# Kernel optimization log

Hardware: AMD Instinct MI355X
Metric: run time of the kernel (lower is better)

Reference implementation:

```python
import jax, jax.numpy as jnp
import numpy as np

ODE_UNFOLDS = 6  # keras-ncp LTCCell default
EPS = 1e-8


def setup_inputs() -> dict:
    dim = 1024
    U = 2 * dim
    B, T = 32, 128
    key = jax.random.key(0)
    ks = jax.random.split(key, 12)
    u = lambda k, shape, lo, hi: jax.random.uniform(k, shape, jnp.float32, lo, hi)
    return {
        "inputs": jax.random.normal(ks[0], (B, T, dim), jnp.float32),
        # per-neuron params (keras-ncp initializer ranges)
        "gleak": u(ks[1], (U,), 0.001, 1.0),
        "vleak": u(ks[2], (U,), -0.2, 0.2),
        "cm": u(ks[3], (U,), 0.4, 0.6),
        # per-synapse params; slot 0 = self synapse, slot 1 = pair synapse (j+dim)%U
        "w": u(ks[4], (U, 2), 0.001, 1.0),
        "sigma": u(ks[5], (U, 2), 3.0, 8.0),
        "mu": u(ks[6], (U, 2), 0.3, 0.8),
        "erev": jnp.full((U, 2), -1.0, jnp.float32),  # internal polarity -1
        # sensory synapse params; each neuron j has one sensory source j%dim
        "sens_w": u(ks[7], (U,), 0.001, 1.0),
        "sens_sigma": u(ks[8], (U,), 3.0, 8.0),
        "sens_mu": u(ks[9], (U,), 0.3, 0.8),
        "sens_erev": jnp.full((U,), 1.0, jnp.float32),  # sensory polarity +1
        # affine input/output maps (LTCCell defaults: ones / zeros)
        "input_w": jnp.ones((dim,), jnp.float32),
        "input_b": jnp.zeros((dim,), jnp.float32),
        "output_w": jnp.ones((dim,), jnp.float32),
        "output_b": jnp.zeros((dim,), jnp.float32),
    }


def reference(inputs, gleak, vleak, cm, w, sigma, mu, erev,
              sens_w, sens_sigma, sens_mu, sens_erev,
              input_w, input_b, output_w, output_b):
    B, T, dim = inputs.shape
    U = 2 * dim
    idx = jnp.arange(U)
    src_idx = jnp.stack([idx, (idx + dim) % U], axis=-1)  # [U,2] recurrent sources per dst
    smod = idx % dim                                       # sensory source per dst

    sp_w = jax.nn.softplus(w)          # [U,2]
    sp_sw = jax.nn.softplus(sens_w)    # [U]
    sp_gleak = jax.nn.softplus(gleak)  # [U]
    cm_t = jax.nn.softplus(cm) * ODE_UNFOLDS  # elapsed_time = 1.0

    def step(v, x_t):
        x = x_t * input_w + input_b                                            # [B,dim]
        s_act = sp_sw * jax.nn.sigmoid((x[:, smod] - sens_mu) * sens_sigma)    # [B,U]
        num_s = s_act * sens_erev
        den_s = s_act
        for _ in range(ODE_UNFOLDS):
            va = v[:, src_idx]                                                  # [B,U,2]
            wa = sp_w * jax.nn.sigmoid((va - mu) * sigma)                      # [B,U,2]
            num = jnp.sum(wa * erev, axis=-1) + num_s                          # [B,U]
            den = jnp.sum(wa, axis=-1) + den_s                                 # [B,U]
            v = (cm_t * v + sp_gleak * vleak + num) / (cm_t + sp_gleak + den + EPS)
        return v, None

    v0 = jnp.zeros((B, U), inputs.dtype)
    v_last, _ = jax.lax.scan(step, v0, jnp.swapaxes(inputs, 0, 1))  # scan over time
    return v_last[:, :dim] * output_w + output_b  # motor neurons + affine output map
```

## Files before the change

### kernel.cpp

```cpp
#include <hip/hip_runtime.h>

#define T_STEPS 128
#define DIM 1024
#define ODE_UNFOLDS 6
#define EPS 1e-8f
#define L2E 1.44269504088896340736f

__device__ __forceinline__ float fexp2(float x) { return __builtin_amdgcn_exp2f(x); }
__device__ __forceinline__ float frcp(float x)  { return __builtin_amdgcn_rcpf(x); }

__device__ __forceinline__ float softplus_init(float x) {
  return log2f(1.0f + exp2f(x * L2E)) * (1.0f / L2E);
}

__device__ __forceinline__ float swap_adj(float x) {
  int y = __builtin_amdgcn_mov_dpp(__float_as_int(x), 0xB1, 0xF, 0xF, true);
  return __int_as_float(y);
}

__global__ __launch_bounds__(256) void memcell_kernel(
    const float* __restrict__ inputs,
    const float* __restrict__ gleak,
    const float* __restrict__ vleak,
    const float* __restrict__ cm,
    const float* __restrict__ w,
    const float* __restrict__ sigma,
    const float* __restrict__ mu,
    const float* __restrict__ erev,
    const float* __restrict__ sens_w,
    const float* __restrict__ sens_sigma,
    const float* __restrict__ sens_mu,
    const float* __restrict__ sens_erev,
    const float* __restrict__ input_w,
    const float* __restrict__ input_b,
    const float* __restrict__ output_w,
    const float* __restrict__ output_b,
    float* __restrict__ out)
{
  const int tid  = blockIdx.x * blockDim.x + threadIdx.x;
  const int p    = tid >> 1;
  const int half = tid & 1;
  const int b    = p >> 10;
  const int col  = p & (DIM - 1);
  const int u    = col + (half << 10);

  const float spw0  = softplus_init(w[2*u]);
  const float spw1  = softplus_init(w[2*u+1]);
  const float e0    = erev[2*u];
  const float e1    = erev[2*u+1];
  const float spw0e = spw0 * e0;
  const float spw1e = spw1 * e1;
  const float sg0   = sigma[2*u],  sg1 = sigma[2*u+1];
  const float mu0   = mu[2*u],     mu1 = mu[2*u+1];
  const float negA0 = -sg0 * L2E,  B0c = mu0 * sg0 * L2E;
  const float negA1 = -sg1 * L2E,  B1c = mu1 * sg1 * L2E;
  const float gl    = softplus_init(gleak[u]);
  const float glv   = gl * vleak[u];
  const float cmt   = softplus_init(cm[u]) * (float)ODE_UNFOLDS;
  const float dbase = cmt + gl + EPS;
  const float spsw  = softplus_init(sens_w[u]);
  const float ssg   = sens_sigma[u];
  const float smu   = sens_mu[u];
  const float negAs = -ssg * L2E,  Bsc = smu * ssg * L2E;
  const float serev = sens_erev[u];
  const float iw    = input_w[col];
  const float ib    = input_b[col];

  const float negA1p = swap_adj(negA1);
  const float B1p    = swap_adj(B1c);

  const float* xp = inputs + ((size_t)b * T_STEPS) * DIM + col;

  float xs0 = xp[0 * DIM];
  float xs1 = xp[1 * DIM];
  float xs2 = xp[2 * DIM];
  float xs3 = xp[3 * DIM];

  float v = 0.0f;

  for (int tb = 0; tb < T_STEPS; tb += 4) {
    const float c0 = xs0, c1 = xs1, c2 = xs2, c3 = xs3;
    if (tb + 4 < T_STEPS) {
      const float* nx = xp + (size_t)(tb + 4) * DIM;
      xs0 = nx[0 * DIM];
      xs1 = nx[1 * DIM];
      xs2 = nx[2 * DIM];
      xs3 = nx[3 * DIM];
    }
    #pragma unroll
    for (int j = 0; j < 4; ++j) {
      const float xr = (j == 0) ? c0 : (j == 1) ? c1 : (j == 2) ? c2 : c3;
      const float x  = fmaf(xr, iw, ib);
      const float ts    = fexp2(fmaf(x, negAs, Bsc));
      const float s     = spsw * frcp(1.0f + ts);
      const float ns    = fmaf(s, serev, glv);
      const float ds    = dbase + s;
      const float dspw0 = ds + spw0;
      #pragma unroll
      for (int k = 0; k < ODE_UNFOLDS; ++k) {
        const float z0  = fmaf(v, negA0,  B0c);
        const float z1p = fmaf(v, negA1p, B1p);
        const float t0  = fexp2(z0);
        const float tp  = fexp2(z1p);
        const float t1  = swap_adj(tp);
        const float a0  = 1.0f + t0;
        const float numerN = fmaf(cmt, v, ns);
        const float q   = fmaf(numerN, a0, spw0e);
        const float e_t = spw1e * a0;
        const float p   = fmaf(ds, t0, dspw0);
        const float s_t = spw1 * a0;
        const float a1  = 1.0f + t1;
        const float nume = fmaf(a1, q, e_t);
        const float deno = fmaf(a1, p, s_t);
        const float r   = frcp(deno);
        v = nume * r;
      }
    }
  }

  if (half == 0) {
    out[(size_t)b * DIM + col] = fmaf(v, output_w[col], output_b[col]);
  }
}

extern "C" void kernel_launch(void* const* d_in, const int* in_sizes, int n_in,
                              void* d_out, int out_size, void* d_ws, size_t ws_size,
                              hipStream_t stream) {
  const float* inputs      = (const float*)d_in[0];
  const float* gleak       = (const float*)d_in[1];
  const float* vleak       = (const float*)d_in[2];
  const float* cm          = (const float*)d_in[3];
  const float* w           = (const float*)d_in[4];
  const float* sigma       = (const float*)d_in[5];
  const float* mu          = (const float*)d_in[6];
  const float* erev        = (const float*)d_in[7];
  const float* sens_w      = (const float*)d_in[8];
  const float* sens_sigma  = (const float*)d_in[9];
  const float* sens_mu     = (const float*)d_in[10];
  const float* sens_erev   = (const float*)d_in[11];
  const float* input_w     = (const float*)d_in[12];
  const float* input_b     = (const float*)d_in[13];
  const float* output_w    = (const float*)d_in[14];
  const float* output_b    = (const float*)d_in[15];

  const int B = in_sizes[0] / (T_STEPS * DIM);
  const int U = 2 * DIM;
  const int total_threads = B * U;
  dim3 block(256);
  dim3 grid(total_threads / 256);

  memcell_kernel<<<grid, block, 0, stream>>>(
      inputs, gleak, vleak, cm, w, sigma, mu, erev,
      sens_w, sens_sigma, sens_mu, sens_erev,
      input_w, input_b, output_w, output_b, (float*)d_out);
}
```

Before: 119.3 us.

## Split each neuron pair across four lanes with one synapse exp per lane

Each column pair now runs on four lanes instead of two. Each lane evaluates a single synapse sigmoid exponential and gets the other synapse's term from its neighbour through a DPP swap. The updated voltage is broadcast within the quad with a quad_perm DPP so each lane picks up its source neuron's voltage. This doubles the thread count to raise per-SIMD occupancy and shorten per-lane exp work on a latency-bound recurrence, at the cost of duplicated per-unit arithmetic and an extra cross-lane move on the dependency chain.

```diff
diff --git a/kernel.cpp b/kernel.cpp
--- a/kernel.cpp
+++ b/kernel.cpp
@@ -15,6 +15,11 @@
 
 __device__ __forceinline__ float swap_adj(float x) {
   int y = __builtin_amdgcn_mov_dpp(__float_as_int(x), 0xB1, 0xF, 0xF, true);
+  return __int_as_float(y);
+}
+
+__device__ __forceinline__ float bcast02(float x) {
+  int y = __builtin_amdgcn_mov_dpp(__float_as_int(x), 0x28, 0xF, 0xF, true);
   return __int_as_float(y);
 }
 
@@ -38,22 +43,21 @@
     float* __restrict__ out)
 {
   const int tid  = blockIdx.x * blockDim.x + threadIdx.x;
-  const int p    = tid >> 1;
-  const int half = tid & 1;
-  const int b    = p >> 10;
-  const int col  = p & (DIM - 1);
+  const int sub  = tid & 3;
+  const int pp   = tid >> 2;
+  const int b    = pp >> 10;
+  const int col  = pp & (DIM - 1);
+  const int half = sub >> 1;
+  const int syn  = sub & 1;
   const int u    = col + (half << 10);
 
-  const float spw0  = softplus_init(w[2*u]);
-  const float spw1  = softplus_init(w[2*u+1]);
-  const float e0    = erev[2*u];
-  const float e1    = erev[2*u+1];
-  const float spw0e = spw0 * e0;
-  const float spw1e = spw1 * e1;
-  const float sg0   = sigma[2*u],  sg1 = sigma[2*u+1];
-  const float mu0   = mu[2*u],     mu1 = mu[2*u+1];
-  const float negA0 = -sg0 * L2E,  B0c = mu0 * sg0 * L2E;
-  const float negA1 = -sg1 * L2E,  B1c = mu1 * sg1 * L2E;
+  const float wOwn  = softplus_init(w[2*u + syn]);
+  const float wRec  = softplus_init(w[2*u + (1 - syn)]);
+  const float wOwnE = wOwn * erev[2*u + syn];
+  const float wRecE = wRec * erev[2*u + (1 - syn)];
+  const float sg    = sigma[2*u + syn];
+  const float muc   = mu[2*u + syn];
+  const float negA  = -sg * L2E, Bc = muc * sg * L2E;
   const float gl    = softplus_init(gleak[u]);
   const float glv   = gl * vleak[u];
   const float cmt   = softplus_init(cm[u]) * (float)ODE_UNFOLDS;
@@ -61,13 +65,10 @@
   const float spsw  = softplus_init(sens_w[u]);
   const float ssg   = sens_sigma[u];
   const float smu   = sens_mu[u];
-  const float negAs = -ssg * L2E,  Bsc = smu * ssg * L2E;
+  const float negAs = -ssg * L2E, Bsc = smu * ssg * L2E;
   const float serev = sens_erev[u];
   const float iw    = input_w[col];
   const float ib    = input_b[col];
-
-  const float negA1p = swap_adj(negA1);
-  const float B1p    = swap_adj(B1c);
 
   const float* xp = inputs + ((size_t)b * T_STEPS) * DIM + col;
 
@@ -76,7 +77,8 @@
   float xs2 = xp[2 * DIM];
   float xs3 = xp[3 * DIM];
 
-  float v = 0.0f;
+  float v_src  = 0.0f;
+  float v_unit = 0.0f;
 
   for (int tb = 0; tb < T_STEPS; tb += 4) {
     const float c0 = xs0, c1 = xs1, c2 = xs2, c3 = xs3;
@@ -95,31 +97,30 @@
       const float s     = spsw * frcp(1.0f + ts);
       const float ns    = fmaf(s, serev, glv);
       const float ds    = dbase + s;
-      const float dspw0 = ds + spw0;
+      const float dsOwn = ds + wOwn;
       #pragma unroll
       for (int k = 0; k < ODE_UNFOLDS; ++k) {
-        const float z0  = fmaf(v, negA0,  B0c);
-        const float z1p = fmaf(v, negA1p, B1p);
-        const float t0  = fexp2(z0);
-        const float tp  = fexp2(z1p);
-        const float t1  = swap_adj(tp);
-        const float a0  = 1.0f + t0;
-        const float numerN = fmaf(cmt, v, ns);
-        const float q   = fmaf(numerN, a0, spw0e);
-        const float e_t = spw1e * a0;
-        const float p   = fmaf(ds, t0, dspw0);
-        const float s_t = spw1 * a0;
-        const float a1  = 1.0f + t1;
-        const float nume = fmaf(a1, q, e_t);
-        const float deno = fmaf(a1, p, s_t);
-        const float r   = frcp(deno);
-        v = nume * r;
+        const float z     = fmaf(v_src, negA, Bc);
+        const float t_own = fexp2(z);
+        const float t_rec = swap_adj(t_own);
+        const float aOwn  = 1.0f + t_own;
+        const float numerN = fmaf(cmt, v_unit, ns);
+        const float q     = fmaf(numerN, aOwn, wOwnE);
+        const float e_    = wRecE * aOwn;
+        const float p     = fmaf(ds, t_own, dsOwn);
+        const float s_    = wRec * aOwn;
+        const float aRec  = 1.0f + t_rec;
+        const float nume  = fmaf(aRec, q, e_);
+        const float deno  = fmaf(aRec, p, s_);
+        const float vN    = nume * frcp(deno);
+        v_unit = vN;
+        v_src  = bcast02(vN);
       }
     }
   }
 
-  if (half == 0) {
-    out[(size_t)b * DIM + col] = fmaf(v, output_w[col], output_b[col]);
+  if (sub == 0) {
+    out[(size_t)b * DIM + col] = fmaf(v_unit, output_w[col], output_b[col]);
   }
 }
 
@@ -145,7 +146,7 @@
 
   const int B = in_sizes[0] / (T_STEPS * DIM);
   const int U = 2 * DIM;
-  const int total_threads = B * U;
+  const int total_threads = 2 * B * U;
   dim3 block(256);
   dim3 grid(total_threads / 256);
 
```

Result: slower. 142.3 us (+19.3%).
